# Optimization experiments

Hardware: AMD Instinct MI355X
Metric: run time of the kernel (lower is better)

The kernel has to match this reference:

```python
import jax, jax.numpy as jnp
import numpy as np

NUM_TOKENS = 16384
D_MODEL = 2048
NUM_EXPERTS = 8
TOP_K = 2


def setup_inputs() -> dict:
    key = jax.random.key(0)
    kx, kw = jax.random.split(key)
    x = jax.random.normal(kx, (NUM_TOKENS, D_MODEL), dtype=jnp.float32)
    # nn.Linear(d_model, num_experts, bias=False): weight shape [num_experts, d_model]
    W = jax.random.normal(kw, (NUM_EXPERTS, D_MODEL), dtype=jnp.float32) * (1.0 / np.sqrt(D_MODEL))
    return {"x": x, "W": W}


def reference(x, W):
    # router logits: [T, E]
    logits = jnp.einsum('td,ed->te', x, W)
    # softmax over experts in float32 (matches dtype=torch.float)
    probs = jax.nn.softmax(logits.astype(jnp.float32), axis=1)
    # top-k experts per token, then renormalize the selected weights
    routing_weights, selected_experts = jax.lax.top_k(probs, TOP_K)  # [T, k]
    routing_weights = routing_weights / jnp.sum(routing_weights, axis=-1, keepdims=True)
    return routing_weights, selected_experts
```

## Files before the change

kernel.cpp:

```cpp
#include <hip/hip_runtime.h>


constexpr int D = 2048;
constexpr int E = 8;
constexpr int NT = 16384;
constexpr int T_PER_WAVE = 4;
constexpr int WAVES_PER_BLOCK = 4;
constexpr int BLOCK = WAVES_PER_BLOCK * 64;
constexpr int CHUNK = 64 * 4;

__global__ __launch_bounds__(BLOCK) void gate_kernel(
    const float* __restrict__ x, const float* __restrict__ W,
    float* __restrict__ out) {
  const int lane = threadIdx.x & 63;
  const int wave = blockIdx.x * WAVES_PER_BLOCK + (threadIdx.x >> 6);
  const int t0 = wave * T_PER_WAVE;

  float acc[T_PER_WAVE][E];
#pragma unroll
  for (int t = 0; t < T_PER_WAVE; t++)
#pragma unroll
    for (int e = 0; e < E; e++) acc[t][e] = 0.f;

  for (int c = 0; c < D / CHUNK; c++) {
    const int k = c * CHUNK + lane * 4;
    float4 xv[T_PER_WAVE];
#pragma unroll
    for (int t = 0; t < T_PER_WAVE; t++)
      xv[t] = *(const float4*)(x + (size_t)(t0 + t) * D + k);
#pragma unroll
    for (int e = 0; e < E; e++) {
      const float4 wv = *(const float4*)(W + (size_t)e * D + k);
#pragma unroll
      for (int t = 0; t < T_PER_WAVE; t++) {
        acc[t][e] += xv[t].x * wv.x;
        acc[t][e] += xv[t].y * wv.y;
        acc[t][e] += xv[t].z * wv.z;
        acc[t][e] += xv[t].w * wv.w;
      }
    }
  }

#pragma unroll
  for (int t = 0; t < T_PER_WAVE; t++)
#pragma unroll
    for (int e = 0; e < E; e++) {
      float v = acc[t][e];
#pragma unroll
      for (int off = 32; off; off >>= 1) v += __shfl_xor(v, off, 64);
      acc[t][e] = v;
    }

  if (lane == 0) {
    float w1v[T_PER_WAVE], w2v[T_PER_WAVE];
    float i1v[T_PER_WAVE], i2v[T_PER_WAVE];
#pragma unroll
    for (int t = 0; t < T_PER_WAVE; t++) {
      float m1 = acc[t][0];
      int i1 = 0;
#pragma unroll
      for (int e = 1; e < E; e++)
        if (acc[t][e] > m1) { m1 = acc[t][e]; i1 = e; }
      float m2 = -INFINITY;
      int i2 = 0;
#pragma unroll
      for (int e = 0; e < E; e++)
        if (e != i1 && acc[t][e] > m2) { m2 = acc[t][e]; i2 = e; }
      const float s = __expf(m2 - m1);
      const float w1 = 1.f / (1.f + s);
      w1v[t] = w1;
      w2v[t] = 1.f - w1;
      i1v[t] = (float)i1;
      i2v[t] = (float)i2;
    }
    float4* ow = (float4*)(out + 2 * (size_t)t0);
    ow[0] = make_float4(w1v[0], w2v[0], w1v[1], w2v[1]);
    ow[1] = make_float4(w1v[2], w2v[2], w1v[3], w2v[3]);
    float4* oi = (float4*)(out + 2 * (size_t)NT + 2 * (size_t)t0);
    oi[0] = make_float4(i1v[0], i2v[0], i1v[1], i2v[1]);
    oi[1] = make_float4(i1v[2], i2v[2], i1v[3], i2v[3]);
  }
}

extern "C" void kernel_launch(void* const* d_in, const int* in_sizes, int n_in,
                              void* d_out, int out_size, void* d_ws,
                              size_t ws_size, hipStream_t stream) {
  const float* x = (const float*)d_in[0];
  const float* W = (const float*)d_in[1];
  float* out = (float*)d_out;
  const int blocks = NT / (T_PER_WAVE * WAVES_PER_BLOCK);
  gate_kernel<<<blocks, BLOCK, 0, stream>>>(x, W, out);
}
```

Before: 193.5 us.

## Use transpose-style butterfly reduction and nontemporal loads for router logits

Replaces 32 independent full-wave shuffle reductions with a halving butterfly that splits the accumulators across lanes, cutting cross-lane shuffle count sharply. Final per-token logits go through shared memory so four lanes each compute top-2 and write outputs. x is loaded with nontemporal hints to avoid polluting cache. Adds select logic and a block-wide barrier.

```diff
diff --git a/kernel.cpp b/kernel.cpp
--- a/kernel.cpp
+++ b/kernel.cpp
@@ -1,4 +1,5 @@
 #include <hip/hip_runtime.h>
+#include <math.h>
 
 
 constexpr int D = 2048;
@@ -8,77 +9,82 @@
 constexpr int WAVES_PER_BLOCK = 4;
 constexpr int BLOCK = WAVES_PER_BLOCK * 64;
 constexpr int CHUNK = 64 * 4;
+constexpr int NV = T_PER_WAVE * E;
+
+typedef float fvec4 __attribute__((ext_vector_type(4)));
 
 __global__ __launch_bounds__(BLOCK) void gate_kernel(
     const float* __restrict__ x, const float* __restrict__ W,
     float* __restrict__ out) {
   const int lane = threadIdx.x & 63;
-  const int wave = blockIdx.x * WAVES_PER_BLOCK + (threadIdx.x >> 6);
+  const int wslot = threadIdx.x >> 6;
+  const int wave = blockIdx.x * WAVES_PER_BLOCK + wslot;
   const int t0 = wave * T_PER_WAVE;
 
-  float acc[T_PER_WAVE][E];
+  float v[NV];
 #pragma unroll
-  for (int t = 0; t < T_PER_WAVE; t++)
-#pragma unroll
-    for (int e = 0; e < E; e++) acc[t][e] = 0.f;
+  for (int i = 0; i < NV; i++) v[i] = 0.f;
 
   for (int c = 0; c < D / CHUNK; c++) {
     const int k = c * CHUNK + lane * 4;
-    float4 xv[T_PER_WAVE];
+    fvec4 xv[T_PER_WAVE];
 #pragma unroll
     for (int t = 0; t < T_PER_WAVE; t++)
-      xv[t] = *(const float4*)(x + (size_t)(t0 + t) * D + k);
+      xv[t] = __builtin_nontemporal_load(
+          (const fvec4*)(x + (size_t)(t0 + t) * D + k));
 #pragma unroll
     for (int e = 0; e < E; e++) {
-      const float4 wv = *(const float4*)(W + (size_t)e * D + k);
+      const fvec4 wv = *(const fvec4*)(W + (size_t)e * D + k);
 #pragma unroll
       for (int t = 0; t < T_PER_WAVE; t++) {
-        acc[t][e] += xv[t].x * wv.x;
-        acc[t][e] += xv[t].y * wv.y;
-        acc[t][e] += xv[t].z * wv.z;
-        acc[t][e] += xv[t].w * wv.w;
+        v[t * E + e] += xv[t].x * wv.x;
+        v[t * E + e] += xv[t].y * wv.y;
+        v[t * E + e] += xv[t].z * wv.z;
+        v[t * E + e] += xv[t].w * wv.w;
       }
     }
   }
 
+  int n = NV / 2;
 #pragma unroll
-  for (int t = 0; t < T_PER_WAVE; t++)
+  for (int o = 32; o >= 2; o >>= 1) {
+    const bool upper = (lane & o) != 0;
 #pragma unroll
-    for (int e = 0; e < E; e++) {
-      float v = acc[t][e];
+    for (int i = 0; i < 16; i++) {
+      if (i < n) {
+        const float send = upper ? v[i] : v[i + n];
+        const float keep = upper ? v[i + n] : v[i];
+        v[i] = keep + __shfl_xor(send, o, 64);
+      }
+    }
+    n >>= 1;
+  }
+  const float r = v[0] + __shfl_xor(v[0], 1, 64);
+
+  __shared__ float red[WAVES_PER_BLOCK][NV];
+  red[wslot][(lane >> 1) & 31] = r;
+  __syncthreads();
+
+  if (lane < T_PER_WAVE) {
+    const int t = lane;
+    float l[E];
 #pragma unroll
-      for (int off = 32; off; off >>= 1) v += __shfl_xor(v, off, 64);
-      acc[t][e] = v;
-    }
-
-  if (lane == 0) {
-    float w1v[T_PER_WAVE], w2v[T_PER_WAVE];
-    float i1v[T_PER_WAVE], i2v[T_PER_WAVE];
+    for (int e = 0; e < E; e++) l[e] = red[wslot][t * E + e];
+    float m1 = l[0];
+    int i1 = 0;
 #pragma unroll
-    for (int t = 0; t < T_PER_WAVE; t++) {
-      float m1 = acc[t][0];
-      int i1 = 0;
+    for (int e = 1; e < E; e++)
+      if (l[e] > m1) { m1 = l[e]; i1 = e; }
+    float m2 = -INFINITY;
+    int i2 = 0;
 #pragma unroll
-      for (int e = 1; e < E; e++)
-        if (acc[t][e] > m1) { m1 = acc[t][e]; i1 = e; }
-      float m2 = -INFINITY;
-      int i2 = 0;
-#pragma unroll
-      for (int e = 0; e < E; e++)
-        if (e != i1 && acc[t][e] > m2) { m2 = acc[t][e]; i2 = e; }
-      const float s = __expf(m2 - m1);
-      const float w1 = 1.f / (1.f + s);
-      w1v[t] = w1;
-      w2v[t] = 1.f - w1;
-      i1v[t] = (float)i1;
-      i2v[t] = (float)i2;
-    }
-    float4* ow = (float4*)(out + 2 * (size_t)t0);
-    ow[0] = make_float4(w1v[0], w2v[0], w1v[1], w2v[1]);
-    ow[1] = make_float4(w1v[2], w2v[2], w1v[3], w2v[3]);
-    float4* oi = (float4*)(out + 2 * (size_t)NT + 2 * (size_t)t0);
-    oi[0] = make_float4(i1v[0], i2v[0], i1v[1], i2v[1]);
-    oi[1] = make_float4(i1v[2], i2v[2], i1v[3], i2v[3]);
+    for (int e = 0; e < E; e++)
+      if (e != i1 && l[e] > m2) { m2 = l[e]; i2 = e; }
+    const float s = __expf(m2 - m1);
+    const float w1 = 1.f / (1.f + s);
+    *(float2*)(out + 2 * (size_t)(t0 + t)) = make_float2(w1, 1.f - w1);
+    *(float2*)(out + 2 * (size_t)NT + 2 * (size_t)(t0 + t)) =
+        make_float2((float)i1, (float)i2);
   }
 }
 
```

Result: slower. 205.4 us (+6.2%).
